# Performance work log

Hardware: AMD Instinct MI355X
Metric: run time of the kernel (lower is better)

The kernel has to match this reference:

```python
import jax, jax.numpy as jnp
import numpy as np

NEG_INF = -1e9  # large negative for masking (avoid NaN rows under -inf with fully masked rows)
LEAKY_SLOPE = 0.2

def setup_inputs() -> dict:
    key = jax.random.key(0)
    k1, k2, k3, k4, k5 = jax.random.split(key, 5)
    N, in_dim, out_dim = 8192, 512, 64
    x = jax.random.normal(k1, (N, in_dim), dtype=jnp.float32)
    adj = jax.random.randint(k2, (N, N), 0, 2, dtype=jnp.int32)
    W = jax.random.normal(k3, (out_dim, in_dim), dtype=jnp.float32) * (1.0 / np.sqrt(in_dim))
    a_src = jax.random.normal(k4, (out_dim,), dtype=jnp.float32)
    a_dst = jax.random.normal(k5, (out_dim,), dtype=jnp.float32)
    return {"x": x, "adj": adj, "W": W, "a_src": a_src, "a_dst": a_dst}

def reference(x, adj, W, a_src, a_dst):
    # Linear projection: Wh[n, d]
    Wh = x @ W.T
    # Additive GAT attention: e[i, j] = LeakyReLU(a_src . Wh_i + a_dst . Wh_j)
    s = Wh @ a_src  # [N]
    d = Wh @ a_dst  # [N]
    e = jax.nn.leaky_relu(s[:, None] + d[None, :], negative_slope=LEAKY_SLOPE)  # [N, N]
    e = jnp.where(adj > 0, e, NEG_INF)
    alpha = jax.nn.softmax(e, axis=1)  # [N, N]
    # Dropout on alpha is identity in eval/reference mode.
    h_prime = alpha @ Wh  # [N, out_dim]
    return h_prime
```

## Files before the change

### kernel.cpp

```cpp
#include <hip/hip_runtime.h>
#include <hip/hip_bf16.h>

#define GN 8192
#define IN_DIM 512
#define ODIM 64
#define SLOPE 0.2f
#define KSPL 4
#define KCOLS (GN / KSPL)
#define KITER (KCOLS / 32)

typedef __attribute__((ext_vector_type(4))) float  f32x4;
typedef __attribute__((ext_vector_type(4))) int    i32x4;
typedef __attribute__((ext_vector_type(8))) short  bf16x8;
typedef __attribute__((ext_vector_type(4))) unsigned short u16x4;

static __device__ __forceinline__ float bf2f(unsigned short u) {
    return __uint_as_float(((unsigned)u) << 16);
}
static __device__ __forceinline__ unsigned short f2bf(float f) {
    union { float f; unsigned u; } c; c.f = f;
    unsigned b = c.u;
    return (unsigned short)((b + 0x7fffu + ((b >> 16) & 1u)) >> 16);
}

static __device__ __forceinline__ bf16x8 load8(const void* p, size_t off, int f32) {
    if (f32) {
        f32x4 lo = *(const f32x4*)((const float*)p + off);
        f32x4 hi = *(const f32x4*)((const float*)p + off + 4);
        bf16x8 r;
        #pragma unroll
        for (int q = 0; q < 4; ++q) {
            r[q]     = (short)f2bf(lo[q]);
            r[4 + q] = (short)f2bf(hi[q]);
        }
        return r;
    }
    return *(const bf16x8*)((const ushort*)p + off);
}

extern "C" __global__ __launch_bounds__(256)
void gat_pack(const int* __restrict__ adj, unsigned* __restrict__ gbm)
{
    const size_t ui = (size_t)blockIdx.x * 256 + threadIdx.x;
    const int* p = adj + ui * 32;
    unsigned w = 0;
    #pragma unroll
    for (int c = 0; c < 8; ++c) {
        i32x4 v = ((const i32x4*)p)[c];
        #pragma unroll
        for (int q = 0; q < 4; ++q)
            w |= (v[q] > 0 ? 1u : 0u) << (c * 4 + q);
    }
    gbm[ui] = w;
}

extern "C" __global__ __launch_bounds__(256)
void gat_proj(const void* __restrict__ x_, const void* __restrict__ W_,
              const void* __restrict__ as_, const void* __restrict__ ad_,
              ushort* __restrict__ WhTp, float* __restrict__ s_arr,
              float* __restrict__ E1, float* __restrict__ E2,
              int* __restrict__ dmax_bits, int* __restrict__ dflag)
{
    const int wave = threadIdx.x >> 6;
    const int lane = threadIdx.x & 63;
    unsigned xw = ((const unsigned*)x_)[lane];
    unsigned ef = (xw >> 23) & 0xffu;
    unsigned long long vt = __ballot(ef > 60u && ef < 180u);
    const int f32 = (__popcll(vt) >= 32) ? 1 : 0;
    if (blockIdx.x == 0 && threadIdx.x == 0) *dflag = f32;

    const int quad = lane >> 4;
    const int lq   = lane & 15;
    const int i0   = blockIdx.x * 64 + wave * 16;

    f32x4 acc[4] = {{0,0,0,0},{0,0,0,0},{0,0,0,0},{0,0,0,0}};
    const size_t arow = (size_t)(i0 + lq) * IN_DIM;
    #pragma unroll 2
    for (int k0 = 0; k0 < IN_DIM; k0 += 32) {
        const int kk = k0 + quad * 8;
        bf16x8 a  = load8(x_, arow + kk, f32);
        bf16x8 b0 = load8(W_, (size_t)( 0 + lq) * IN_DIM + kk, f32);
        bf16x8 b1 = load8(W_, (size_t)(16 + lq) * IN_DIM + kk, f32);
        bf16x8 b2 = load8(W_, (size_t)(32 + lq) * IN_DIM + kk, f32);
        bf16x8 b3 = load8(W_, (size_t)(48 + lq) * IN_DIM + kk, f32);
        acc[0] = __builtin_amdgcn_mfma_f32_16x16x32_bf16(a, b0, acc[0], 0, 0, 0);
        acc[1] = __builtin_amdgcn_mfma_f32_16x16x32_bf16(a, b1, acc[1], 0, 0, 0);
        acc[2] = __builtin_amdgcn_mfma_f32_16x16x32_bf16(a, b2, acc[2], 0, 0, 0);
        acc[3] = __builtin_amdgcn_mfma_f32_16x16x32_bf16(a, b3, acc[3], 0, 0, 0);
    }
    float av_s[4], av_d[4];
    #pragma unroll
    for (int t = 0; t < 4; ++t) {
        const int n = t * 16 + lq;
        av_s[t] = f32 ? ((const float*)as_)[n] : bf2f(((const ushort*)as_)[n]);
        av_d[t] = f32 ? ((const float*)ad_)[n] : bf2f(((const ushort*)ad_)[n]);
    }
    #pragma unroll
    for (int t = 0; t < 4; ++t) {
        u16x4 pk;
        #pragma unroll
        for (int r = 0; r < 4; ++r) pk[r] = f2bf(acc[t][r]);
        const size_t hw = ((size_t)((i0 >> 3) + (quad >> 1)) * 64 + t * 16 + lq) * 8
                          + (quad & 1) * 4;
        *(u16x4*)(WhTp + hw) = pk;
    }
    float ps[4], pd[4];
    #pragma unroll
    for (int r = 0; r < 4; ++r) {
        float s = 0.f, d = 0.f;
        #pragma unroll
        for (int t = 0; t < 4; ++t) {
            s = fmaf(acc[t][r], av_s[t], s);
            d = fmaf(acc[t][r], av_d[t], d);
        }
        #pragma unroll
        for (int off = 1; off < 16; off <<= 1) {
            s += __shfl_xor(s, off);
            d += __shfl_xor(d, off);
        }
        ps[r] = s; pd[r] = d;
    }
    if (lq == 0) {
        float dmx = -1e30f;
        #pragma unroll
        for (int r = 0; r < 4; ++r) {
            const int n = i0 + quad * 4 + r;
            const float dv = pd[r];
            s_arr[n] = ps[r];
            E1[n] = __expf(fminf(dv, 87.f));
            E2[n] = __expf(SLOPE * dv);
            dmx = fmaxf(dmx, dv);
        }
        if (dmx > 0.f) atomicMax(dmax_bits, __float_as_int(dmx));
    }
}

extern "C" __global__ __launch_bounds__(256, 2)
void gat_attn(const unsigned char* __restrict__ gbm,
              const ushort* __restrict__ WhTp,
              const float* __restrict__ s_arr,
              const float* __restrict__ E1, const float* __restrict__ E2,
              const int* __restrict__ dmax_bits,
              float* __restrict__ part, float* __restrict__ prs)
{
    __shared__ float lE[2 * KCOLS];
    const int b    = blockIdx.x;
    const int ib   = b & 127;
    const int js0  = b >> 7;
    const int wave = threadIdx.x >> 6;
    const int lane = threadIdx.x & 63;
    const int quad = lane >> 4;
    const int lq   = lane & 15;
    const int i0   = ib * 64;
    const int i    = i0 + wave * 16 + lq;
    const int colbase = js0 * KCOLS;

    {
        const int m0 = threadIdx.x * 8;
        *(f32x4*)&lE[m0]              = *(const f32x4*)(E1 + colbase + m0);
        *(f32x4*)&lE[m0 + 4]          = *(const f32x4*)(E1 + colbase + m0 + 4);
        *(f32x4*)&lE[KCOLS + m0]      = *(const f32x4*)(E2 + colbase + m0);
        *(f32x4*)&lE[KCOLS + m0 + 4]  = *(const f32x4*)(E2 + colbase + m0 + 4);
    }

    const float dmax = __int_as_float(*dmax_bits);
    const float si  = s_arr[i];
    const float tbv = si + dmax;
    const float mi  = fmaxf(tbv, SLOPE * tbv);
    const float Aw  = __expf(si - mi);
    const float Bw  = __expf(SLOPE * si - mi);

    const unsigned char* mrow = gbm + (size_t)i * (GN / 8);

    f32x4 acc0 = {0,0,0,0}, acc1 = {0,0,0,0}, acc2 = {0,0,0,0}, acc3 = {0,0,0,0};
    f32x4 acc4 = {0,0,0,0};
    bf16x8 ones;
    #pragma unroll
    for (int q = 0; q < 8; ++q) ones[q] = (short)0x3F80;

    unsigned bm = *(const unsigned*)(mrow + (colbase >> 3));
    bf16x8 b0, b1, b2, b3;
    {
        const ushort* nb = WhTp + ((size_t)(colbase >> 3) + quad) * 512;
        b0 = *(const bf16x8*)(nb + ( 0 + lq) * 8);
        b1 = *(const bf16x8*)(nb + (16 + lq) * 8);
        b2 = *(const bf16x8*)(nb + (32 + lq) * 8);
        b3 = *(const bf16x8*)(nb + (48 + lq) * 8);
    }
    __syncthreads();

    #pragma unroll 4
    for (int u = 0; u < KITER; ++u) {
        const int un   = (u < KITER - 1) ? u + 1 : u;
        const int ncol = colbase + un * 32;
        const unsigned nbm = *(const unsigned*)(mrow + (ncol >> 3));
        const ushort* nb = WhTp + ((size_t)(ncol >> 3) + quad) * 512;
        const bf16x8 nb0 = *(const bf16x8*)(nb + ( 0 + lq) * 8);
        const bf16x8 nb1 = *(const bf16x8*)(nb + (16 + lq) * 8);
        const bf16x8 nb2 = *(const bf16x8*)(nb + (32 + lq) * 8);
        const bf16x8 nb3 = *(const bf16x8*)(nb + (48 + lq) * 8);
        const float* pe = lE + u * 32 + quad * 8;
        const f32x4 e1a = *(const f32x4*)pe;
        const f32x4 e1b = *(const f32x4*)(pe + 4);
        const f32x4 e2a = *(const f32x4*)(pe + KCOLS);
        const f32x4 e2b = *(const f32x4*)(pe + KCOLS + 4);
        const unsigned m8 = (bm >> (quad * 8)) & 0xffu;
        float w[8];
        #pragma unroll
        for (int q = 0; q < 4; ++q) {
            const float w0 = fmaxf(Aw * e1a[q], Bw * e2a[q]);
            const float w1 = fmaxf(Aw * e1b[q], Bw * e2b[q]);
            w[q]     = ((m8 >> q) & 1u) ? w0 : 0.f;
            w[4 + q] = ((m8 >> (4 + q)) & 1u) ? w1 : 0.f;
        }
        union { bf16x8 v; __hip_bfloat162 h[4]; } af;
        #pragma unroll
        for (int q = 0; q < 4; ++q)
            af.h[q] = __float22bfloat162_rn(make_float2(w[2 * q], w[2 * q + 1]));
        acc0 = __builtin_amdgcn_mfma_f32_16x16x32_bf16(af.v, b0, acc0, 0, 0, 0);
        acc1 = __builtin_amdgcn_mfma_f32_16x16x32_bf16(af.v, b1, acc1, 0, 0, 0);
        acc2 = __builtin_amdgcn_mfma_f32_16x16x32_bf16(af.v, b2, acc2, 0, 0, 0);
        acc3 = __builtin_amdgcn_mfma_f32_16x16x32_bf16(af.v, b3, acc3, 0, 0, 0);
        acc4 = __builtin_amdgcn_mfma_f32_16x16x32_bf16(af.v, ones, acc4, 0, 0, 0);
        bm = nbm; b0 = nb0; b1 = nb1; b2 = nb2; b3 = nb3;
    }

    const int orow = i0 + wave * 16 + quad * 4;
    float* pslab = part + ((size_t)js0 * GN + orow) * ODIM;
    if (lq == 0) {
        #pragma unroll
        for (int r = 0; r < 4; ++r) prs[js0 * GN + orow + r] = acc4[r];
    }
    #pragma unroll
    for (int r = 0; r < 4; ++r) {
        pslab[r * ODIM +  0 + lq] = acc0[r];
        pslab[r * ODIM + 16 + lq] = acc1[r];
        pslab[r * ODIM + 32 + lq] = acc2[r];
        pslab[r * ODIM + 48 + lq] = acc3[r];
    }
}

extern "C" __global__ __launch_bounds__(256)
void gat_final(const float* __restrict__ part, const float* __restrict__ prs,
               const int* __restrict__ flag, void* __restrict__ out)
{
    const int idx = blockIdx.x * 256 + threadIdx.x;
    const int row = idx >> 6;
    float a = 0.f, s = 0.f;
    #pragma unroll
    for (int k = 0; k < KSPL; ++k) {
        a += part[(size_t)k * GN * ODIM + idx];
        s += prs[k * GN + row];
    }
    const float v = a / s;
    if (*flag) ((float*)out)[idx] = v;
    else       ((ushort*)out)[idx] = f2bf(v);
}

extern "C" void kernel_launch(void* const* d_in, const int* in_sizes, int n_in,
                              void* d_out, int out_size, void* d_ws, size_t ws_size,
                              hipStream_t stream)
{
    const void* x     = d_in[0];
    const int*  adj   = (const int*)d_in[1];
    const void* W     = d_in[2];
    const void* a_src = d_in[3];
    const void* a_dst = d_in[4];

    char* ws = (char*)d_ws;
    size_t off = 0;
    int* dmax_bits = (int*)(ws + off);  off += 128;
    int* dflag = (int*)(ws + off);      off += 128;
    size_t zero_bytes = off;
    float* s_arr = (float*)(ws + off);  off += (size_t)GN * 4;
    float* E1    = (float*)(ws + off);  off += (size_t)GN * 4;
    float* E2    = (float*)(ws + off);  off += (size_t)GN * 4;
    ushort* WhTp = (ushort*)(ws + off); off += (size_t)ODIM * GN * 2;
    unsigned* gbm = (unsigned*)(ws + off); off += (size_t)GN * (GN / 8);
    float* part  = (float*)(ws + off);  off += (size_t)KSPL * GN * ODIM * 4;
    float* prs   = (float*)(ws + off);  off += (size_t)KSPL * GN * 4;

    hipMemsetAsync(ws, 0, zero_bytes, stream);
    gat_pack<<<GN * (GN / 32) / 256, 256, 0, stream>>>(adj, gbm);
    gat_proj<<<GN / 64, 256, 0, stream>>>(x, W, a_src, a_dst,
                                          WhTp, s_arr, E1, E2, dmax_bits, dflag);
    gat_attn<<<128 * KSPL, 256, 0, stream>>>((const unsigned char*)gbm, WhTp,
                                             s_arr, E1, E2, dmax_bits,
                                             part, prs);
    gat_final<<<GN * ODIM / 256, 256, 0, stream>>>(part, prs, dflag, d_out);
}
```

Before: 455.2 us.

## Fuse adjacency bitpacking into attention kernel and stage Wh tiles in LDS

Removes the separate gat_pack kernel and its bitmask buffer. Each attention block now reads its 64x512 slice of the int32 adjacency directly and packs it into an LDS byte mask. The block also stages its column tile of WhT into shared memory. KSPL grows from 4 to 16, giving 2048 blocks with smaller column chunks, and the register prefetch pipeline is dropped. The aim is to avoid the extra write and read of the packed mask and one kernel launch. In exchange, LDS use per block rises to about 73 KB, which limits occupancy, and the partial-sum buffers and the final reduction grow fourfold.

```diff
diff --git a/kernel.cpp b/kernel.cpp
--- a/kernel.cpp
+++ b/kernel.cpp
@@ -5,9 +5,10 @@
 #define IN_DIM 512
 #define ODIM 64
 #define SLOPE 0.2f
-#define KSPL 4
-#define KCOLS (GN / KSPL)
-#define KITER (KCOLS / 32)
+#define KSPL 16
+#define CB (GN / KSPL)
+#define CITER (CB / 32)
+#define LSTRIDE 68
 
 typedef __attribute__((ext_vector_type(4))) float  f32x4;
 typedef __attribute__((ext_vector_type(4))) int    i32x4;
@@ -36,22 +37,6 @@
         return r;
     }
     return *(const bf16x8*)((const ushort*)p + off);
-}
-
-extern "C" __global__ __launch_bounds__(256)
-void gat_pack(const int* __restrict__ adj, unsigned* __restrict__ gbm)
-{
-    const size_t ui = (size_t)blockIdx.x * 256 + threadIdx.x;
-    const int* p = adj + ui * 32;
-    unsigned w = 0;
-    #pragma unroll
-    for (int c = 0; c < 8; ++c) {
-        i32x4 v = ((const i32x4*)p)[c];
-        #pragma unroll
-        for (int q = 0; q < 4; ++q)
-            w |= (v[q] > 0 ? 1u : 0u) << (c * 4 + q);
-    }
-    gbm[ui] = w;
 }
 
 extern "C" __global__ __launch_bounds__(256)
@@ -135,32 +120,53 @@
     }
 }
 
-extern "C" __global__ __launch_bounds__(256, 2)
-void gat_attn(const unsigned char* __restrict__ gbm,
-              const ushort* __restrict__ WhTp,
+extern "C" __global__ __launch_bounds__(256)
+void gat_attn(const int* __restrict__ adj, const ushort* __restrict__ WhTp,
               const float* __restrict__ s_arr,
               const float* __restrict__ E1, const float* __restrict__ E2,
               const int* __restrict__ dmax_bits,
               float* __restrict__ part, float* __restrict__ prs)
 {
-    __shared__ float lE[2 * KCOLS];
+    __shared__ ushort lB[CB * 64];
+    __shared__ float  lE[2 * CB];
+    __shared__ unsigned char mb[64 * LSTRIDE];
+
     const int b    = blockIdx.x;
-    const int ib   = b & 127;
-    const int js0  = b >> 7;
+    const int ib   = b >> 4;
+    const int js   = b & 15;
     const int wave = threadIdx.x >> 6;
     const int lane = threadIdx.x & 63;
     const int quad = lane >> 4;
     const int lq   = lane & 15;
     const int i0   = ib * 64;
     const int i    = i0 + wave * 16 + lq;
-    const int colbase = js0 * KCOLS;
+    const int colbase = js * CB;
 
     {
-        const int m0 = threadIdx.x * 8;
-        *(f32x4*)&lE[m0]              = *(const f32x4*)(E1 + colbase + m0);
-        *(f32x4*)&lE[m0 + 4]          = *(const f32x4*)(E1 + colbase + m0 + 4);
-        *(f32x4*)&lE[KCOLS + m0]      = *(const f32x4*)(E2 + colbase + m0);
-        *(f32x4*)&lE[KCOLS + m0 + 4]  = *(const f32x4*)(E2 + colbase + m0 + 4);
+        const f32x4* src = (const f32x4*)(WhTp + (size_t)(colbase >> 3) * 512);
+        f32x4* dst = (f32x4*)lB;
+        #pragma unroll
+        for (int c = 0; c < 16; ++c)
+            dst[c * 256 + threadIdx.x] = src[c * 256 + threadIdx.x];
+    }
+    if (threadIdx.x < 128)
+        ((f32x4*)lE)[threadIdx.x] = ((const f32x4*)(E1 + colbase))[threadIdx.x];
+    else
+        ((f32x4*)(lE + CB))[threadIdx.x - 128] =
+            ((const f32x4*)(E2 + colbase))[threadIdx.x - 128];
+    #pragma unroll
+    for (int rr = 0; rr < 16; ++rr) {
+        const int li2 = wave * 16 + rr;
+        const int* p = adj + (size_t)(i0 + li2) * GN + colbase + lane * 8;
+        const i32x4 va = ((const i32x4*)p)[0];
+        const i32x4 vb = ((const i32x4*)p)[1];
+        unsigned byte = 0;
+        #pragma unroll
+        for (int q = 0; q < 4; ++q) {
+            byte |= (va[q] > 0 ? 1u : 0u) << q;
+            byte |= (vb[q] > 0 ? 1u : 0u) << (4 + q);
+        }
+        mb[li2 * LSTRIDE + lane] = (unsigned char)byte;
     }
 
     const float dmax = __int_as_float(*dmax_bits);
@@ -170,41 +176,29 @@
     const float Aw  = __expf(si - mi);
     const float Bw  = __expf(SLOPE * si - mi);
 
-    const unsigned char* mrow = gbm + (size_t)i * (GN / 8);
-
     f32x4 acc0 = {0,0,0,0}, acc1 = {0,0,0,0}, acc2 = {0,0,0,0}, acc3 = {0,0,0,0};
     f32x4 acc4 = {0,0,0,0};
     bf16x8 ones;
     #pragma unroll
     for (int q = 0; q < 8; ++q) ones[q] = (short)0x3F80;
 
-    unsigned bm = *(const unsigned*)(mrow + (colbase >> 3));
-    bf16x8 b0, b1, b2, b3;
-    {
-        const ushort* nb = WhTp + ((size_t)(colbase >> 3) + quad) * 512;
-        b0 = *(const bf16x8*)(nb + ( 0 + lq) * 8);
-        b1 = *(const bf16x8*)(nb + (16 + lq) * 8);
-        b2 = *(const bf16x8*)(nb + (32 + lq) * 8);
-        b3 = *(const bf16x8*)(nb + (48 + lq) * 8);
-    }
     __syncthreads();
 
+    const int li = wave * 16 + lq;
     #pragma unroll 4
-    for (int u = 0; u < KITER; ++u) {
-        const int un   = (u < KITER - 1) ? u + 1 : u;
-        const int ncol = colbase + un * 32;
-        const unsigned nbm = *(const unsigned*)(mrow + (ncol >> 3));
-        const ushort* nb = WhTp + ((size_t)(ncol >> 3) + quad) * 512;
-        const bf16x8 nb0 = *(const bf16x8*)(nb + ( 0 + lq) * 8);
-        const bf16x8 nb1 = *(const bf16x8*)(nb + (16 + lq) * 8);
-        const bf16x8 nb2 = *(const bf16x8*)(nb + (32 + lq) * 8);
-        const bf16x8 nb3 = *(const bf16x8*)(nb + (48 + lq) * 8);
+    for (int u = 0; u < CITER; ++u) {
+        const unsigned bw = *(const unsigned*)&mb[li * LSTRIDE + u * 4];
+        const ushort* bb = lB + (size_t)(u * 4 + quad) * 512;
+        const bf16x8 b0 = *(const bf16x8*)(bb + ( 0 + lq) * 8);
+        const bf16x8 b1 = *(const bf16x8*)(bb + (16 + lq) * 8);
+        const bf16x8 b2 = *(const bf16x8*)(bb + (32 + lq) * 8);
+        const bf16x8 b3 = *(const bf16x8*)(bb + (48 + lq) * 8);
         const float* pe = lE + u * 32 + quad * 8;
         const f32x4 e1a = *(const f32x4*)pe;
         const f32x4 e1b = *(const f32x4*)(pe + 4);
-        const f32x4 e2a = *(const f32x4*)(pe + KCOLS);
-        const f32x4 e2b = *(const f32x4*)(pe + KCOLS + 4);
-        const unsigned m8 = (bm >> (quad * 8)) & 0xffu;
+        const f32x4 e2a = *(const f32x4*)(pe + CB);
+        const f32x4 e2b = *(const f32x4*)(pe + CB + 4);
+        const unsigned m8 = (bw >> (quad * 8)) & 0xffu;
         float w[8];
         #pragma unroll
         for (int q = 0; q < 4; ++q) {
@@ -222,14 +216,13 @@
         acc2 = __builtin_amdgcn_mfma_f32_16x16x32_bf16(af.v, b2, acc2, 0, 0, 0);
         acc3 = __builtin_amdgcn_mfma_f32_16x16x32_bf16(af.v, b3, acc3, 0, 0, 0);
         acc4 = __builtin_amdgcn_mfma_f32_16x16x32_bf16(af.v, ones, acc4, 0, 0, 0);
-        bm = nbm; b0 = nb0; b1 = nb1; b2 = nb2; b3 = nb3;
     }
 
     const int orow = i0 + wave * 16 + quad * 4;
-    float* pslab = part + ((size_t)js0 * GN + orow) * ODIM;
+    float* pslab = part + ((size_t)js * GN + orow) * ODIM;
     if (lq == 0) {
         #pragma unroll
-        for (int r = 0; r < 4; ++r) prs[js0 * GN + orow + r] = acc4[r];
+        for (int r = 0; r < 4; ++r) prs[js * GN + orow + r] = acc4[r];
     }
     #pragma unroll
     for (int r = 0; r < 4; ++r) {
@@ -276,16 +269,13 @@
     float* E1    = (float*)(ws + off);  off += (size_t)GN * 4;
     float* E2    = (float*)(ws + off);  off += (size_t)GN * 4;
     ushort* WhTp = (ushort*)(ws + off); off += (size_t)ODIM * GN * 2;
-    unsigned* gbm = (unsigned*)(ws + off); off += (size_t)GN * (GN / 8);
     float* part  = (float*)(ws + off);  off += (size_t)KSPL * GN * ODIM * 4;
     float* prs   = (float*)(ws + off);  off += (size_t)KSPL * GN * 4;
 
     hipMemsetAsync(ws, 0, zero_bytes, stream);
-    gat_pack<<<GN * (GN / 32) / 256, 256, 0, stream>>>(adj, gbm);
     gat_proj<<<GN / 64, 256, 0, stream>>>(x, W, a_src, a_dst,
                                           WhTp, s_arr, E1, E2, dmax_bits, dflag);
-    gat_attn<<<128 * KSPL, 256, 0, stream>>>((const unsigned char*)gbm, WhTp,
-                                             s_arr, E1, E2, dmax_bits,
-                                             part, prs);
+    gat_attn<<<128 * KSPL, 256, 0, stream>>>(adj, WhTp, s_arr, E1, E2,
+                                             dmax_bits, part, prs);
     gat_final<<<GN * ODIM / 256, 256, 0, stream>>>(part, prs, dflag, d_out);
 }
```

New measurement: 437.7 us. -3.8%, faster.
